# Kernel tuning notes

Hardware: AMD Instinct MI355X
Metric: run time of the kernel (lower is better)

Reference implementation:

```python
import jax, jax.numpy as jnp
import numpy as np

B, T, C = 2, 2048, 2048
N_HEAD, N_KV = 32, 8
HD = C // N_HEAD  # 64
N_REP = N_HEAD // N_KV  # 4
ROPE_BASE = 10000.0


def setup_inputs() -> dict:
    key = jax.random.key(0)
    ks = jax.random.split(key, 5)
    s = 0.02
    return {
        "x": jax.random.normal(ks[0], (B, T, C), jnp.float32),
        "Wq": jax.random.normal(ks[1], (C, N_HEAD * HD), jnp.float32) * s,
        "Wk": jax.random.normal(ks[2], (C, N_KV * HD), jnp.float32) * s,
        "Wv": jax.random.normal(ks[3], (C, N_KV * HD), jnp.float32) * s,
        "Wo": jax.random.normal(ks[4], (N_HEAD * HD, C), jnp.float32) * s,
    }


def _rope_cos_sin(seq_len, head_dim, dtype):
    inv_freq = 1.0 / (ROPE_BASE ** (jnp.arange(0, head_dim, 2, dtype=jnp.float32) / head_dim))
    t = jnp.arange(seq_len, dtype=jnp.float32)
    freqs = t[:, None] * inv_freq[None, :]           # (T, hd/2)
    emb = jnp.concatenate([freqs, freqs], axis=-1)    # (T, hd)
    return jnp.cos(emb).astype(dtype), jnp.sin(emb).astype(dtype)


def _rotate_half(x):
    h = x.shape[-1] // 2
    return jnp.concatenate([-x[..., h:], x[..., :h]], axis=-1)


def reference(x, Wq, Wk, Wv, Wo):
    b, t, c = x.shape
    # projections -> (B, H, T, hd)
    q = (x @ Wq).reshape(b, t, N_HEAD, HD).transpose(0, 2, 1, 3)
    k = (x @ Wk).reshape(b, t, N_KV, HD).transpose(0, 2, 1, 3)
    v = (x @ Wv).reshape(b, t, N_KV, HD).transpose(0, 2, 1, 3)

    cos, sin = _rope_cos_sin(t, HD, x.dtype)          # (T, hd)
    q = q * cos + _rotate_half(q) * sin
    k = k * cos + _rotate_half(k) * sin

    # GQA: group query heads (B, n_kv, n_rep, T, hd) against shared KV (no repeat materialization)
    qg = q.reshape(b, N_KV, N_REP, t, HD)
    scale = 1.0 / jnp.sqrt(jnp.asarray(HD, x.dtype))
    scores = jnp.einsum('bgrqd,bgkd->bgrqk', qg, k) * scale  # (B, n_kv, n_rep, T, T)
    causal = jnp.tril(jnp.ones((t, t), bool))
    scores = jnp.where(causal, scores, jnp.asarray(-jnp.inf, scores.dtype))
    probs = jax.nn.softmax(scores, axis=-1)
    out = jnp.einsum('bgrqk,bgkd->bgrqd', probs, v)          # (B, n_kv, n_rep, T, hd)
    out = out.reshape(b, N_HEAD, t, HD).transpose(0, 2, 1, 3).reshape(b, t, N_HEAD * HD)
    return out @ Wo
```

## Files before the change

### kernel.cpp

```cpp
#include <hip/hip_runtime.h>
#include <stdint.h>

#define Bn 2
#define Tn 2048
#define Cn 2048
#define NHEAD 32
#define NKVH 8
#define HDIM 64
#define Mn (Bn*Tn)
#define NQKV 3072
#define KOFF 2048
#define VOFF 2560

typedef __attribute__((ext_vector_type(8))) short bf16x8;
typedef __attribute__((ext_vector_type(4))) float f32x4;

#define AS1 __attribute__((address_space(1)))
#define AS3 __attribute__((address_space(3)))
#define GLOAD_LDS16(g, l) __builtin_amdgcn_global_load_lds((const AS1 void*)(g), (AS3 void*)(l), 16, 0, 0)

#define SCL 0.18033688f

#define SYNC_FENCE() __builtin_amdgcn_sched_barrier(0)
#define WAIT_VM8()  do { asm volatile("s_waitcnt vmcnt(8)" ::: "memory"); SYNC_FENCE(); } while (0)
#define WAIT_VM0()  do { asm volatile("s_waitcnt vmcnt(0)" ::: "memory"); SYNC_FENCE(); } while (0)
#define BARRIER_RAW() do { __builtin_amdgcn_s_barrier(); SYNC_FENCE(); } while (0)

__device__ __forceinline__ unsigned short f2bf(float f) {
    union { float f; unsigned u; } v; v.f = f;
    return (unsigned short)((v.u + 0x7fffu + ((v.u >> 16) & 1u)) >> 16);
}
__device__ __forceinline__ float bf2f(unsigned short b) {
    union { unsigned u; float f; } v; v.u = ((unsigned)b) << 16;
    return v.f;
}

__global__ void convert_f32_bf16(const float* __restrict__ src,
                                 unsigned short* __restrict__ dst, int n4) {
    int i = blockIdx.x * blockDim.x + threadIdx.x;
    if (i >= n4) return;
    float4 f = ((const float4*)src)[i];
    ushort4 o;
    o.x = f2bf(f.x); o.y = f2bf(f.y); o.z = f2bf(f.z); o.w = f2bf(f.w);
    ((ushort4*)dst)[i] = o;
}

__global__ void transpose_convert(const float* __restrict__ src,
                                  unsigned short* __restrict__ dst, int K, int N) {
    __shared__ float tile[32][33];
    int k0 = blockIdx.x * 32, n0 = blockIdx.y * 32;
    int tx = threadIdx.x, ty = threadIdx.y;
    #pragma unroll
    for (int yy = 0; yy < 32; yy += 8)
        tile[ty + yy][tx] = src[(size_t)(k0 + ty + yy) * N + n0 + tx];
    __syncthreads();
    #pragma unroll
    for (int yy = 0; yy < 32; yy += 8)
        dst[(size_t)(n0 + ty + yy) * K + k0 + tx] = f2bf(tile[tx][ty + yy]);
}

__global__ void transpose_wqkv(const float* __restrict__ Wq, const float* __restrict__ Wk,
                               const float* __restrict__ Wv, unsigned short* __restrict__ dst) {
    __shared__ float tile[32][33];
    int k0 = blockIdx.x * 32, n0 = blockIdx.y * 32;
    const float* src; int srcN, c0;
    if (n0 < 2048)      { src = Wq; srcN = 2048; c0 = n0; }
    else if (n0 < 2560) { src = Wk; srcN = 512;  c0 = n0 - 2048; }
    else                { src = Wv; srcN = 512;  c0 = n0 - 2560; }
    int tx = threadIdx.x, ty = threadIdx.y;
    #pragma unroll
    for (int yy = 0; yy < 32; yy += 8)
        tile[ty + yy][tx] = src[(size_t)(k0 + ty + yy) * srcN + c0 + tx];
    __syncthreads();
    #pragma unroll
    for (int yy = 0; yy < 32; yy += 8)
        dst[(size_t)(n0 + ty + yy) * Cn + k0 + tx] = f2bf(tile[tx][ty + yy]);
}

__global__ void rope_tables(float* __restrict__ ct, float* __restrict__ st) {
    int i = blockIdx.x * blockDim.x + threadIdx.x;
    int t = i >> 5, d = i & 31;
    float invf = powf(10000.0f, -(float)d / 32.0f);
    float f = (float)t * invf;
    ct[i] = cosf(f);
    st[i] = sinf(f);
}

__global__ void transpose_v(const unsigned short* __restrict__ qkv,
                            unsigned short* __restrict__ vt) {
    __shared__ unsigned short tile[32][33];
    int t0 = blockIdx.x * 32;
    int b = blockIdx.y >> 3, kvh = blockIdx.y & 7;
    int d0 = blockIdx.z * 32;
    int tx = threadIdx.x, ty = threadIdx.y;
    #pragma unroll
    for (int yy = 0; yy < 32; yy += 8)
        tile[ty + yy][tx] = qkv[(size_t)(b * Tn + t0 + ty + yy) * NQKV + VOFF + kvh * 64 + d0 + tx];
    __syncthreads();
    #pragma unroll
    for (int yy = 0; yy < 32; yy += 8)
        vt[(size_t)((b * 8 + kvh) * 64 + d0 + ty + yy) * Tn + t0 + tx] = tile[tx][ty + yy];
}

template <int BM, int BN, int WMv, int WNv, bool ROPE, bool SWZ>
__global__ __launch_bounds__(WMv * WNv * 64, 2) void gemm_pipe(
    const unsigned short* __restrict__ A, const unsigned short* __restrict__ Bt,
    unsigned short* __restrict__ outb, float* __restrict__ outf, int N, int K,
    const float* __restrict__ ct, const float* __restrict__ st) {
    constexpr int THREADS = WMv * WNv * 64;
    constexpr int MR = BM / WMv / 16;
    constexpr int NR = BN / WNv / 16;
    constexpr int LOADS = (BM * 64 * 2) / (THREADS * 16);

    __shared__ unsigned short sA[2][BM * 64];
    __shared__ unsigned short sB[2][BN * 64];

    int tid = threadIdx.x;
    int wid = tid >> 6, lane = tid & 63;
    int wm = wid / WNv, wn = wid % WNv;
    int g = lane >> 4, r16 = lane & 15;

    int bx, by;
    if (SWZ) {
        int nwg = gridDim.x * gridDim.y;
        int lid = blockIdx.y * gridDim.x + blockIdx.x;
        int swz = (lid & 7) * (nwg >> 3) + (lid >> 3);
        bx = swz % gridDim.x; by = swz / gridDim.x;
    } else {
        bx = blockIdx.x; by = blockIdx.y;
    }
    int brow = by * BM, bcol = bx * BN;

    int NT = K / 64;

    auto stage = [&](int kt, int b) {
        #pragma unroll
        for (int li = 0; li < LOADS; li++) {
            int cb = li * (THREADS * 16) + wid * 1024;
            int bo = cb + lane * 16;
            int row = bo >> 7;
            int coff = (bo & 127) ^ ((row & 7) << 4);
            GLOAD_LDS16(A + (size_t)(brow + row) * K + kt * 64 + (coff >> 1),
                        (char*)&sA[b][0] + cb);
            GLOAD_LDS16(Bt + (size_t)(bcol + row) * K + kt * 64 + (coff >> 1),
                        (char*)&sB[b][0] + cb);
        }
    };

    f32x4 acc[MR][NR];
    #pragma unroll
    for (int m = 0; m < MR; m++)
        #pragma unroll
        for (int n = 0; n < NR; n++) acc[m][n] = (f32x4){0.f, 0.f, 0.f, 0.f};

    stage(0, 0);
    stage(1, 1);

    for (int kt = 0; kt < NT; kt++) {
        if (kt + 1 < NT) { WAIT_VM8(); } else { WAIT_VM0(); }
        BARRIER_RAW();
        const char* cA = (const char*)&sA[kt & 1][0];
        const char* cB = (const char*)&sB[kt & 1][0];
        bf16x8 av[MR][2];
        #pragma unroll
        for (int m = 0; m < MR; m++)
            #pragma unroll
            for (int kc = 0; kc < 2; kc++) {
                int row = wm * (MR * 16) + m * 16 + r16;
                int byo = (row * 128 + kc * 64 + g * 16) ^ ((row & 7) << 4);
                av[m][kc] = *(const bf16x8*)(cA + byo);
            }
        #pragma unroll
        for (int n = 0; n < NR; n++) {
            bf16x8 bv[2];
            #pragma unroll
            for (int kc = 0; kc < 2; kc++) {
                int row = wn * (NR * 16) + n * 16 + r16;
                int byo = (row * 128 + kc * 64 + g * 16) ^ ((row & 7) << 4);
                bv[kc] = *(const bf16x8*)(cB + byo);
            }
            __builtin_amdgcn_s_setprio(1);
            #pragma unroll
            for (int m = 0; m < MR; m++)
                #pragma unroll
                for (int kc = 0; kc < 2; kc++)
                    acc[m][n] = __builtin_amdgcn_mfma_f32_16x16x32_bf16(av[m][kc], bv[kc], acc[m][n], 0, 0, 0);
            __builtin_amdgcn_s_setprio(0);
        }
        BARRIER_RAW();
        if (kt + 2 < NT) stage(kt + 2, kt & 1);
        SYNC_FENCE();
    }

    if (ROPE) {
        #pragma unroll
        for (int m = 0; m < MR; m++) {
            #pragma unroll
            for (int n = 0; n < NR / 2; n++) {
                int col = bcol + wn * (NR * 16) + n * 16 + r16;
                int p = col & 63;
                bool isV = (col >= VOFF);
                float scl = (col < KOFF) ? SCL : 1.0f;
                #pragma unroll
                for (int r = 0; r < 4; r++) {
                    int row = brow + wm * (MR * 16) + m * 16 + g * 4 + r;
                    int tt = row & (Tn - 1);
                    float v0 = acc[m][n][r], v1 = acc[m][n + NR / 2][r];
                    float o0, o1;
                    if (isV) { o0 = v0; o1 = v1; }
                    else {
                        float c = ct[tt * 32 + p], s = st[tt * 32 + p];
                        o0 = (v0 * c - v1 * s) * scl;
                        o1 = (v1 * c + v0 * s) * scl;
                    }
                    outb[(size_t)row * N + col]      = f2bf(o0);
                    outb[(size_t)row * N + col + 32] = f2bf(o1);
                }
            }
        }
    } else {
        #pragma unroll
        for (int m = 0; m < MR; m++) {
            #pragma unroll
            for (int n = 0; n < NR; n++) {
                int row0 = brow + wm * (MR * 16) + m * 16 + g * 4;
                int col = bcol + wn * (NR * 16) + n * 16 + r16;
                #pragma unroll
                for (int r = 0; r < 4; r++)
                    outf[(size_t)(row0 + r) * N + col] = acc[m][n][r];
            }
        }
    }
}

__device__ __forceinline__ void flash_step(
    const bf16x8 (&qf)[2], float (&pl)[4], f32x4 (&oo)[4],
    const unsigned short* __restrict__ sK, const unsigned short* __restrict__ sVt,
    unsigned short* __restrict__ sPw, int g, int r16, int wid, bool masked) {
    f32x4 s[4];
    __builtin_amdgcn_s_setprio(1);
    #pragma unroll
    for (int n = 0; n < 4; n++) {
        s[n] = (f32x4){0.f, 0.f, 0.f, 0.f};
        #pragma unroll
        for (int kc = 0; kc < 2; kc++) {
            int kv = n * 16 + r16;
            int bo = (kv * 128 + kc * 64 + g * 16) ^ ((kv & 7) << 4);
            bf16x8 kf = *(const bf16x8*)((const char*)sK + bo);
            s[n] = __builtin_amdgcn_mfma_f32_16x16x32_bf16(qf[kc], kf, s[n], 0, 0, 0);
        }
    }
    __builtin_amdgcn_s_setprio(0);
    if (masked) {
        #pragma unroll
        for (int n = 0; n < 4; n++)
            #pragma unroll
            for (int r = 0; r < 4; r++)
                s[n][r] = (n * 16 + r16 <= wid * 16 + g * 4 + r) ? s[n][r] : -1e30f;
    }
    #pragma unroll
    for (int n = 0; n < 4; n++)
        #pragma unroll
        for (int r = 0; r < 4; r++) s[n][r] = exp2f(s[n][r]);
    #pragma unroll
    for (int r = 0; r < 4; r++)
        pl[r] += (s[0][r] + s[1][r]) + (s[2][r] + s[3][r]);
    #pragma unroll
    for (int n = 0; n < 4; n++)
        #pragma unroll
        for (int r = 0; r < 4; r++) {
            int prow = g * 4 + r;
            int bo = (prow * 128 + (n * 16 + r16) * 2) ^ ((prow & 7) << 4);
            union { float f; unsigned u; } pv; pv.f = s[n][r];
            *(unsigned short*)((char*)sPw + bo) = (unsigned short)(pv.u >> 16);
        }
    __builtin_amdgcn_s_setprio(1);
    #pragma unroll
    for (int dt = 0; dt < 4; dt++) {
        #pragma unroll
        for (int kc = 0; kc < 2; kc++) {
            int bo = (r16 * 128 + kc * 64 + g * 16) ^ ((r16 & 7) << 4);
            bf16x8 pf = *(const bf16x8*)((const char*)sPw + bo);
            int dd = dt * 16 + r16;
            int bo2 = (dd * 128 + kc * 64 + g * 16) ^ ((dd & 7) << 4);
            bf16x8 vf = *(const bf16x8*)((const char*)sVt + bo2);
            oo[dt] = __builtin_amdgcn_mfma_f32_16x16x32_bf16(pf, vf, oo[dt], 0, 0, 0);
        }
    }
    __builtin_amdgcn_s_setprio(0);
}

__global__ __launch_bounds__(256, 4) void attn_fwd(
    const unsigned short* __restrict__ qkv, const unsigned short* __restrict__ vt,
    unsigned short* __restrict__ att) {
    __shared__ unsigned short sK[2][64 * 64];
    __shared__ unsigned short sVt[2][64 * 64];
    __shared__ unsigned short sP[4][16 * 64];

    int tid = threadIdx.x;
    int wid = tid >> 6, lane = tid & 63;
    int g = lane >> 4, r16 = lane & 15;
    int qp = blockIdx.x;
    int bh = blockIdx.y;
    int b = bh >> 5, qh = bh & 31, kvh = qh >> 2;
    int qtA = qp, qtB = 31 - qp;

    const unsigned short* base = qkv + (size_t)b * Tn * NQKV;
    const unsigned short* kg = base + KOFF + kvh * 64;
    const unsigned short* vg = vt + (size_t)((b * 8 + kvh) * 64) * Tn;

    bf16x8 qfA[2], qfB[2];
    {
        int qrA = qtA * 64 + wid * 16 + r16;
        int qrB = qtB * 64 + wid * 16 + r16;
        #pragma unroll
        for (int kc = 0; kc < 2; kc++) {
            qfA[kc] = *(const bf16x8*)(base + (size_t)qrA * NQKV + qh * 64 + kc * 32 + g * 8);
            qfB[kc] = *(const bf16x8*)(base + (size_t)qrB * NQKV + qh * 64 + kc * 32 + g * 8);
        }
    }

    float plA[4], plB[4];
    f32x4 oA[4], oB[4];
    #pragma unroll
    for (int r = 0; r < 4; r++) { plA[r] = 0.f; plB[r] = 0.f; }
    #pragma unroll
    for (int d = 0; d < 4; d++) {
        oA[d] = (f32x4){0.f, 0.f, 0.f, 0.f};
        oB[d] = (f32x4){0.f, 0.f, 0.f, 0.f};
    }

    unsigned short* sPw = &sP[wid][0];

    #pragma unroll
    for (int jj = 0; jj < 2; jj++) {
        int c = wid * 2 + jj;
        int bo = c * 1024 + lane * 16;
        int row = bo >> 7;
        int coff = (bo & 127) ^ ((row & 7) << 4);
        GLOAD_LDS16(kg + (size_t)row * NQKV + (coff >> 1), (char*)&sK[0][0] + c * 1024);
        GLOAD_LDS16(vg + (size_t)row * Tn + (coff >> 1), (char*)&sVt[0][0] + c * 1024);
    }
    __syncthreads();

    int cur = 0;
    for (int j = 0; j <= qtB; j++) {
        if (j < qtB) {
            int nxt = cur ^ 1;
            #pragma unroll
            for (int jj = 0; jj < 2; jj++) {
                int c = wid * 2 + jj;
                int bo = c * 1024 + lane * 16;
                int row = bo >> 7;
                int coff = (bo & 127) ^ ((row & 7) << 4);
                GLOAD_LDS16(kg + (size_t)((j + 1) * 64 + row) * NQKV + (coff >> 1),
                            (char*)&sK[nxt][0] + c * 1024);
                GLOAD_LDS16(vg + (size_t)row * Tn + (j + 1) * 64 + (coff >> 1),
                            (char*)&sVt[nxt][0] + c * 1024);
            }
        }
        const unsigned short* sKc = &sK[cur][0];
        const unsigned short* sVc = &sVt[cur][0];
        if (j <= qtA) flash_step(qfA, plA, oA, sKc, sVc, sPw, g, r16, wid, j == qtA);
        flash_step(qfB, plB, oB, sKc, sVc, sPw, g, r16, wid, j == qtB);
        __syncthreads();
        cur ^= 1;
    }

    float lA[4], lB[4];
    #pragma unroll
    for (int r = 0; r < 4; r++) {
        float vA = plA[r], vB = plB[r];
        #pragma unroll
        for (int msk = 1; msk < 16; msk <<= 1) {
            vA += __shfl_xor(vA, msk, 64);
            vB += __shfl_xor(vB, msk, 64);
        }
        lA[r] = 1.0f / vA;
        lB[r] = 1.0f / vB;
    }
    #pragma unroll
    for (int dt = 0; dt < 4; dt++)
        #pragma unroll
        for (int r = 0; r < 4; r++) {
            int qgA = qtA * 64 + wid * 16 + g * 4 + r;
            int qgB = qtB * 64 + wid * 16 + g * 4 + r;
            att[(size_t)(b * Tn + qgA) * Cn + qh * 64 + dt * 16 + r16] = f2bf(oA[dt][r] * lA[r]);
            att[(size_t)(b * Tn + qgB) * Cn + qh * 64 + dt * 16 + r16] = f2bf(oB[dt][r] * lB[r]);
        }
}

extern "C" void kernel_launch(void* const* d_in, const int* in_sizes, int n_in,
                              void* d_out, int out_size, void* d_ws, size_t ws_size,
                              hipStream_t stream) {
    const float* x  = (const float*)d_in[0];
    const float* Wq = (const float*)d_in[1];
    const float* Wk = (const float*)d_in[2];
    const float* Wv = (const float*)d_in[3];
    const float* Wo = (const float*)d_in[4];
    float* out = (float*)d_out;

    char* w = (char*)d_ws;
    unsigned short* Xb    = (unsigned short*)w; w += (size_t)Mn * Cn * 2;
    unsigned short* Wqkvt = (unsigned short*)w; w += (size_t)NQKV * Cn * 2;
    unsigned short* Wot   = (unsigned short*)w; w += (size_t)Cn * Cn * 2;
    unsigned short* QKV   = (unsigned short*)w; w += (size_t)Mn * NQKV * 2;
    unsigned short* ATT   = (unsigned short*)w; w += (size_t)Mn * Cn * 2;
    unsigned short* Vt    = (unsigned short*)w; w += (size_t)Bn * NKVH * HDIM * Tn * 2;
    float* ct = (float*)w; w += (size_t)Tn * 32 * 4;
    float* st = (float*)w; w += (size_t)Tn * 32 * 4;

    convert_f32_bf16<<<(Mn * Cn / 4) / 256, 256, 0, stream>>>(x, Xb, Mn * Cn / 4);
    dim3 tb(32, 8);
    transpose_wqkv<<<dim3(64, 96), tb, 0, stream>>>(Wq, Wk, Wv, Wqkvt);
    transpose_convert<<<dim3(64, 64), tb, 0, stream>>>(Wo, Wot, Cn, 2048);
    rope_tables<<<(Tn * 32) / 256, 256, 0, stream>>>(ct, st);

    gemm_pipe<256, 256, 2, 4, true, true><<<dim3(NQKV / 256, Mn / 256), 512, 0, stream>>>(
        Xb, Wqkvt, QKV, nullptr, NQKV, Cn, ct, st);
    transpose_v<<<dim3(Tn / 32, Bn * NKVH, 2), tb, 0, stream>>>(QKV, Vt);
    attn_fwd<<<dim3(16, Bn * NHEAD), 256, 0, stream>>>(QKV, Vt, ATT);
    gemm_pipe<128, 128, 2, 2, false, false><<<dim3(Cn / 128, Mn / 128), 256, 0, stream>>>(
        ATT, Wot, nullptr, out, Cn, Cn, nullptr, nullptr);
}
```

Baseline: 224.7 us.

## Retile QKV GEMM to 256x192 and move RoPE out of GEMM epilogue

The QKV projection GEMM changes from 256x256 tiles (12x16 = 192 blocks, swizzled) to 256x192 tiles (16x16 = 256 blocks, unswizzled). This presumably fills the 256 compute units better. Because a 192-wide tile no longer holds the paired halves of a head, the RoPE epilogue is removed from the GEMM. RoPE for K now runs in a separate small kernel that reads and writes the QKV buffer in place. RoPE plus scaling for Q is fused into the attention kernel's Q fragment load. The cost is an extra kernel launch with a read-modify-write of K, and extra cos/sin table loads per attention block.

```diff
diff --git a/kernel.cpp b/kernel.cpp
--- a/kernel.cpp
+++ b/kernel.cpp
@@ -22,8 +22,7 @@
 #define SCL 0.18033688f
 
 #define SYNC_FENCE() __builtin_amdgcn_sched_barrier(0)
-#define WAIT_VM8()  do { asm volatile("s_waitcnt vmcnt(8)" ::: "memory"); SYNC_FENCE(); } while (0)
-#define WAIT_VM0()  do { asm volatile("s_waitcnt vmcnt(0)" ::: "memory"); SYNC_FENCE(); } while (0)
+#define WAIT_VM_N(N_) do { asm volatile("s_waitcnt vmcnt(" #N_ ")" ::: "memory"); SYNC_FENCE(); } while (0)
 #define BARRIER_RAW() do { __builtin_amdgcn_s_barrier(); SYNC_FENCE(); } while (0)
 
 __device__ __forceinline__ unsigned short f2bf(float f) {
@@ -86,6 +85,21 @@
     st[i] = sinf(f);
 }
 
+__global__ void rope_k(unsigned short* __restrict__ qkv,
+                       const float* __restrict__ ct, const float* __restrict__ st) {
+    int i = blockIdx.x * blockDim.x + threadIdx.x;
+    int p = i & 31;
+    int kvh = (i >> 5) & 7;
+    int bt = i >> 8;
+    int t = bt & (Tn - 1);
+    size_t base = (size_t)bt * NQKV + KOFF + kvh * 64;
+    float v0 = bf2f(qkv[base + p]);
+    float v1 = bf2f(qkv[base + p + 32]);
+    float c = ct[t * 32 + p], s = st[t * 32 + p];
+    qkv[base + p]      = f2bf(v0 * c - v1 * s);
+    qkv[base + p + 32] = f2bf(v1 * c + v0 * s);
+}
+
 __global__ void transpose_v(const unsigned short* __restrict__ qkv,
                             unsigned short* __restrict__ vt) {
     __shared__ unsigned short tile[32][33];
@@ -102,15 +116,15 @@
         vt[(size_t)((b * 8 + kvh) * 64 + d0 + ty + yy) * Tn + t0 + tx] = tile[tx][ty + yy];
 }
 
-template <int BM, int BN, int WMv, int WNv, bool ROPE, bool SWZ>
+template <int BM, int BN, int WMv, int WNv, bool BF16OUT, bool SWZ>
 __global__ __launch_bounds__(WMv * WNv * 64, 2) void gemm_pipe(
     const unsigned short* __restrict__ A, const unsigned short* __restrict__ Bt,
-    unsigned short* __restrict__ outb, float* __restrict__ outf, int N, int K,
-    const float* __restrict__ ct, const float* __restrict__ st) {
+    unsigned short* __restrict__ outb, float* __restrict__ outf, int N, int K) {
     constexpr int THREADS = WMv * WNv * 64;
     constexpr int MR = BM / WMv / 16;
     constexpr int NR = BN / WNv / 16;
-    constexpr int LOADS = (BM * 64 * 2) / (THREADS * 16);
+    constexpr int LA = (BM * 64 * 2) / (THREADS * 16);
+    constexpr int LB = (BN * 64 * 2) / (THREADS * 16);
 
     __shared__ unsigned short sA[2][BM * 64];
     __shared__ unsigned short sB[2][BN * 64];
@@ -135,13 +149,20 @@
 
     auto stage = [&](int kt, int b) {
         #pragma unroll
-        for (int li = 0; li < LOADS; li++) {
+        for (int li = 0; li < LA; li++) {
             int cb = li * (THREADS * 16) + wid * 1024;
             int bo = cb + lane * 16;
             int row = bo >> 7;
             int coff = (bo & 127) ^ ((row & 7) << 4);
             GLOAD_LDS16(A + (size_t)(brow + row) * K + kt * 64 + (coff >> 1),
                         (char*)&sA[b][0] + cb);
+        }
+        #pragma unroll
+        for (int li = 0; li < LB; li++) {
+            int cb = li * (THREADS * 16) + wid * 1024;
+            int bo = cb + lane * 16;
+            int row = bo >> 7;
+            int coff = (bo & 127) ^ ((row & 7) << 4);
             GLOAD_LDS16(Bt + (size_t)(bcol + row) * K + kt * 64 + (coff >> 1),
                         (char*)&sB[b][0] + cb);
         }
@@ -157,7 +178,11 @@
     stage(1, 1);
 
     for (int kt = 0; kt < NT; kt++) {
-        if (kt + 1 < NT) { WAIT_VM8(); } else { WAIT_VM0(); }
+        if (kt + 1 < NT) {
+            if (LA + LB == 8) { WAIT_VM_N(8); } else { WAIT_VM_N(7); }
+        } else {
+            WAIT_VM_N(0);
+        }
         BARRIER_RAW();
         const char* cA = (const char*)&sA[kt & 1][0];
         const char* cB = (const char*)&sB[kt & 1][0];
@@ -192,41 +217,17 @@
         SYNC_FENCE();
     }
 
-    if (ROPE) {
-        #pragma unroll
-        for (int m = 0; m < MR; m++) {
-            #pragma unroll
-            for (int n = 0; n < NR / 2; n++) {
-                int col = bcol + wn * (NR * 16) + n * 16 + r16;
-                int p = col & 63;
-                bool isV = (col >= VOFF);
-                float scl = (col < KOFF) ? SCL : 1.0f;
-                #pragma unroll
-                for (int r = 0; r < 4; r++) {
-                    int row = brow + wm * (MR * 16) + m * 16 + g * 4 + r;
-                    int tt = row & (Tn - 1);
-                    float v0 = acc[m][n][r], v1 = acc[m][n + NR / 2][r];
-                    float o0, o1;
-                    if (isV) { o0 = v0; o1 = v1; }
-                    else {
-                        float c = ct[tt * 32 + p], s = st[tt * 32 + p];
-                        o0 = (v0 * c - v1 * s) * scl;
-                        o1 = (v1 * c + v0 * s) * scl;
-                    }
-                    outb[(size_t)row * N + col]      = f2bf(o0);
-                    outb[(size_t)row * N + col + 32] = f2bf(o1);
-                }
-            }
-        }
-    } else {
-        #pragma unroll
-        for (int m = 0; m < MR; m++) {
-            #pragma unroll
-            for (int n = 0; n < NR; n++) {
-                int row0 = brow + wm * (MR * 16) + m * 16 + g * 4;
-                int col = bcol + wn * (NR * 16) + n * 16 + r16;
-                #pragma unroll
-                for (int r = 0; r < 4; r++)
+    #pragma unroll
+    for (int m = 0; m < MR; m++) {
+        #pragma unroll
+        for (int n = 0; n < NR; n++) {
+            int row0 = brow + wm * (MR * 16) + m * 16 + g * 4;
+            int col = bcol + wn * (NR * 16) + n * 16 + r16;
+            #pragma unroll
+            for (int r = 0; r < 4; r++) {
+                if (BF16OUT)
+                    outb[(size_t)(row0 + r) * N + col] = f2bf(acc[m][n][r]);
+                else
                     outf[(size_t)(row0 + r) * N + col] = acc[m][n][r];
             }
         }
@@ -292,7 +293,8 @@
 
 __global__ __launch_bounds__(256, 4) void attn_fwd(
     const unsigned short* __restrict__ qkv, const unsigned short* __restrict__ vt,
-    unsigned short* __restrict__ att) {
+    unsigned short* __restrict__ att,
+    const float* __restrict__ ct, const float* __restrict__ st) {
     __shared__ unsigned short sK[2][64 * 64];
     __shared__ unsigned short sVt[2][64 * 64];
     __shared__ unsigned short sP[4][16 * 64];
@@ -310,14 +312,24 @@
     const unsigned short* vg = vt + (size_t)((b * 8 + kvh) * 64) * Tn;
 
     bf16x8 qfA[2], qfB[2];
-    {
-        int qrA = qtA * 64 + wid * 16 + r16;
-        int qrB = qtB * 64 + wid * 16 + r16;
-        #pragma unroll
-        for (int kc = 0; kc < 2; kc++) {
-            qfA[kc] = *(const bf16x8*)(base + (size_t)qrA * NQKV + qh * 64 + kc * 32 + g * 8);
-            qfB[kc] = *(const bf16x8*)(base + (size_t)qrB * NQKV + qh * 64 + kc * 32 + g * 8);
-        }
+    int qrA = qtA * 64 + wid * 16 + r16;
+    int qrB = qtB * 64 + wid * 16 + r16;
+    #pragma unroll
+    for (int kc = 0; kc < 2; kc++) {
+        qfA[kc] = *(const bf16x8*)(base + (size_t)qrA * NQKV + qh * 64 + kc * 32 + g * 8);
+        qfB[kc] = *(const bf16x8*)(base + (size_t)qrB * NQKV + qh * 64 + kc * 32 + g * 8);
+    }
+    #pragma unroll
+    for (int e = 0; e < 8; e++) {
+        int p = g * 8 + e;
+        float cA = ct[qrA * 32 + p], sA_ = st[qrA * 32 + p];
+        float a0 = bf2f((unsigned short)qfA[0][e]), a1 = bf2f((unsigned short)qfA[1][e]);
+        qfA[0][e] = (short)f2bf((a0 * cA - a1 * sA_) * SCL);
+        qfA[1][e] = (short)f2bf((a1 * cA + a0 * sA_) * SCL);
+        float cB = ct[qrB * 32 + p], sB_ = st[qrB * 32 + p];
+        float b0 = bf2f((unsigned short)qfB[0][e]), b1 = bf2f((unsigned short)qfB[1][e]);
+        qfB[0][e] = (short)f2bf((b0 * cB - b1 * sB_) * SCL);
+        qfB[1][e] = (short)f2bf((b1 * cB + b0 * sB_) * SCL);
     }
 
     float plA[4], plB[4];
@@ -416,10 +428,11 @@
     transpose_convert<<<dim3(64, 64), tb, 0, stream>>>(Wo, Wot, Cn, 2048);
     rope_tables<<<(Tn * 32) / 256, 256, 0, stream>>>(ct, st);
 
-    gemm_pipe<256, 256, 2, 4, true, true><<<dim3(NQKV / 256, Mn / 256), 512, 0, stream>>>(
-        Xb, Wqkvt, QKV, nullptr, NQKV, Cn, ct, st);
+    gemm_pipe<256, 192, 2, 4, true, false><<<dim3(NQKV / 192, Mn / 256), 512, 0, stream>>>(
+        Xb, Wqkvt, QKV, nullptr, NQKV, Cn);
+    rope_k<<<(Mn * 8 * 32) / 256, 256, 0, stream>>>(QKV, ct, st);
     transpose_v<<<dim3(Tn / 32, Bn * NKVH, 2), tb, 0, stream>>>(QKV, Vt);
-    attn_fwd<<<dim3(16, Bn * NHEAD), 256, 0, stream>>>(QKV, Vt, ATT);
+    attn_fwd<<<dim3(16, Bn * NHEAD), 256, 0, stream>>>(QKV, Vt, ATT, ct, st);
     gemm_pipe<128, 128, 2, 2, false, false><<<dim3(Cn / 128, Mn / 128), 256, 0, stream>>>(
-        ATT, Wot, nullptr, out, Cn, Cn, nullptr, nullptr);
-}
+        ATT, Wot, nullptr, out, Cn, Cn);
+}
```

After: 213.3 us, median of 15. -5.1%, faster.
